# Performance work log

Hardware: AMD Instinct MI355X
Metric: run time of the kernel (lower is better)

Reference implementation:

```python
import jax, jax.numpy as jnp
import numpy as np

B, N, D, H = 4, 2048, 128, 8
DFF = 4 * D
EPS = 1e-5


def _mha(q, k, v, wq, bq, wk, bk, wv, bv, wo, bo):
    # q: [B, Nq, D], k/v: [B, Nk, D]
    b, nq, d = q.shape
    dh = d // H
    qh = (q @ wq + bq).reshape(b, nq, H, dh)
    kh = (k @ wk + bk).reshape(b, k.shape[1], H, dh)
    vh = (v @ wv + bv).reshape(b, v.shape[1], H, dh)
    scores = jnp.einsum('bqhd,bkhd->bhqk', qh, kh) / jnp.sqrt(jnp.float32(dh))
    attn = jax.nn.softmax(scores, axis=-1)
    out = jnp.einsum('bhqk,bkhd->bqhd', attn, vh).reshape(b, nq, d)
    return out @ wo + bo


def _ln(x, g, b):
    m = x.mean(-1, keepdims=True)
    v = x.var(-1, keepdims=True)
    return (x - m) / jnp.sqrt(v + EPS) * g + b


def setup_inputs() -> dict:
    key = jax.random.key(0)
    ks = jax.random.split(key, 20)
    w = lambda k, s: jax.random.normal(k, s, jnp.float32) * 0.02
    inp = {'h': jax.random.normal(ks[0], (B, N, D), jnp.float32)}
    inp['l_idx'] = jnp.arange(N // 2, dtype=jnp.int32)
    inp['b_idx'] = jnp.arange(N // 2, N, dtype=jnp.int32)
    i = 1
    for p in ('sa', 'l2b', 'b2l'):
        for proj in ('q', 'k', 'v', 'o'):
            inp[f'{p}_w{proj}'] = w(ks[i], (D, D)); i += 1
            inp[f'{p}_b{proj}'] = jnp.zeros((D,), jnp.float32)
    inp['ff_w1'] = w(ks[i], (D, DFF)); i += 1
    inp['ff_b1'] = jnp.zeros((DFF,), jnp.float32)
    inp['ff_w2'] = w(ks[i], (DFF, D)); i += 1
    inp['ff_b2'] = jnp.zeros((D,), jnp.float32)
    inp['n1_g'] = jnp.ones((D,), jnp.float32)
    inp['n1_b'] = jnp.zeros((D,), jnp.float32)
    inp['n2_g'] = jnp.ones((D,), jnp.float32)
    inp['n2_b'] = jnp.zeros((D,), jnp.float32)
    return inp


def reference(h, l_idx, b_idx,
              sa_wq, sa_bq, sa_wk, sa_bk, sa_wv, sa_bv, sa_wo, sa_bo,
              l2b_wq, l2b_bq, l2b_wk, l2b_bk, l2b_wv, l2b_bv, l2b_wo, l2b_bo,
              b2l_wq, b2l_bq, b2l_wk, b2l_bk, b2l_wv, b2l_bv, b2l_wo, b2l_bo,
              ff_w1, ff_b1, ff_w2, ff_b2, n1_g, n1_b, n2_g, n2_b):
    # Self-attention over all nodes.
    h_sa = _mha(h, h, h, sa_wq, sa_bq, sa_wk, sa_bk, sa_wv, sa_bv, sa_wo, sa_bo)
    # Gather node-type subsets, cross-attend, scatter into a zero buffer.
    h_l = h[:, l_idx]  # [B, Nl, D]
    h_b = h[:, b_idx]  # [B, Nb, D]
    out_l = _mha(h_l, h_b, h_b, l2b_wq, l2b_bq, l2b_wk, l2b_bk, l2b_wv, l2b_bv, l2b_wo, l2b_bo)
    out_b = _mha(h_b, h_l, h_l, b2l_wq, b2l_bq, b2l_wk, b2l_bk, b2l_wv, b2l_bv, b2l_wo, b2l_bo)
    h_het = jnp.zeros_like(h).at[:, l_idx].set(out_l).at[:, b_idx].set(out_b)
    x = _ln(h + h_sa + h_het, n1_g, n1_b)
    x = jnp.nan_to_num(x, nan=0.0)
    ff = jnp.maximum(x @ ff_w1 + ff_b1, 0.0) @ ff_w2 + ff_b2
    x = _ln(x + ff, n2_g, n2_b)
    return jnp.nan_to_num(x, nan=0.0)
```

## Files before the change

### kernel.cpp

```cpp
#include <hip/hip_runtime.h>

typedef unsigned short u16;
typedef short s16x4 __attribute__((ext_vector_type(4)));
typedef short short8 __attribute__((ext_vector_type(8)));
typedef __bf16 bf16x8 __attribute__((ext_vector_type(8)));
typedef float f32x4 __attribute__((ext_vector_type(4)));
typedef float f32x2 __attribute__((ext_vector_type(2)));
typedef float f32x16 __attribute__((ext_vector_type(16)));

#define DEV static __device__ __forceinline__

DEV u16 f2b(float f){
  union { float f; unsigned u; } v; v.f = f;
  return (u16)((v.u + 0x7fffu + ((v.u >> 16) & 1u)) >> 16);
}

DEV f32x4 mfma16(short8 a, short8 b, f32x4 c){
  return __builtin_amdgcn_mfma_f32_16x16x32_bf16(
      __builtin_bit_cast(bf16x8, a), __builtin_bit_cast(bf16x8, b), c, 0, 0, 0);
}

DEV f32x16 mfma32(short8 a, short8 b, f32x16 c){
  return __builtin_amdgcn_mfma_f32_32x32x16_bf16(
      __builtin_bit_cast(bf16x8, a), __builtin_bit_cast(bf16x8, b), c, 0, 0, 0);
}

DEV short8 ld8(const u16* p){ return *(const short8*)p; }

#if __has_builtin(__builtin_amdgcn_exp2f)
DEV float fexp2(float x){ return __builtin_amdgcn_exp2f(x); }
#else
DEV float fexp2(float x){ return exp2f(x); }
#endif

#define LOG2E 1.44269504088896341f

struct WConvArgs { const float* w[12]; const float* w1; const float* w2; const float* h; u16* dst; u16* hb; };
__global__ __launch_bounds__(256) void k_convert_w(WConvArgs a){
  int i = blockIdx.x*256 + threadIdx.x;
  if (i >= 1376256) return;
  if (i >= 327680){ int j = i - 327680; a.hb[j] = f2b(a.h[j]); return; }
  float v;
  if (i < 196608){ int w = i >> 14, rem = i & 16383, c = rem >> 7, k = rem & 127; v = a.w[w][k*128 + c]; }
  else if (i < 262144){ int rem = i - 196608, c = rem >> 7, k = rem & 127; v = a.w1[k*512 + c]; }
  else { int rem = i - 262144, c = rem >> 9, k = rem & 511; v = a.w2[k*128 + c]; }
  a.dst[i] = f2b(v);
}

struct ProjDesc {
  const u16* Wt; const float* bias; u16* dst;
  int lg_rpb, row_off, vtrans, tile_end; float scale;
};
struct ProjArgs { ProjDesc d[9]; const u16* X; };
__global__ __launch_bounds__(256) void k_qkv(ProjArgs A){
  int wave = (blockIdx.x << 2) + (threadIdx.x >> 6);
  int lane = threadIdx.x & 63;
  int j = 0, base = 0;
  #pragma unroll
  for (int t = 0; t < 8; ++t)
    if (wave >= A.d[t].tile_end){ j = t + 1; base = A.d[t].tile_end; }
  ProjDesc d = A.d[j];
  int local = wave - base;
  int ch = local & 1, rt = local >> 1;
  int lrow = lane & 15, lgrp = lane >> 4, kb = lgrp << 3;
  int rpb_m1 = (1 << d.lg_rpb) - 1;
  int nq = rpb_m1 + 1;
  int rA = (rt << 5) + lrow, rB = rA + 16;
  int gA = ((rA >> d.lg_rpb) << 11) + (rA & rpb_m1) + d.row_off;
  int gB = ((rB >> d.lg_rpb) << 11) + (rB & rpb_m1) + d.row_off;
  const u16* xpA = A.X + (size_t)gA*128 + kb;
  const u16* xpB = A.X + (size_t)gB*128 + kb;
  short8 aA0 = ld8(xpA), aA1 = ld8(xpA+32), aA2 = ld8(xpA+64), aA3 = ld8(xpA+96);
  short8 aB0 = ld8(xpB), aB1 = ld8(xpB+32), aB2 = ld8(xpB+64), aB3 = ld8(xpB+96);
  int rr0base = rt << 5;
  int b_of = rr0base >> d.lg_rpb;
  int q0_ = rr0base & rpb_m1;
  int blk = q0_ >> 5;
  int lgrp2 = ((lgrp & 1) << 1) | (lgrp >> 1);
  #pragma unroll
  for (int cc = 0; cc < 4; ++cc){
    int c = (ch << 6) + (cc << 4) + lrow;
    const u16* wp = d.Wt + c*128 + kb;
    short8 w0 = ld8(wp), w1 = ld8(wp+32), w2 = ld8(wp+64), w3 = ld8(wp+96);
    f32x4 accA = {0.f,0.f,0.f,0.f}, accB = {0.f,0.f,0.f,0.f};
    accA = mfma16(aA0, w0, accA); accB = mfma16(aB0, w0, accB);
    accA = mfma16(aA1, w1, accA); accB = mfma16(aB1, w1, accB);
    accA = mfma16(aA2, w2, accA); accB = mfma16(aB2, w2, accB);
    accA = mfma16(aA3, w3, accA); accB = mfma16(aB3, w3, accB);
    float bv = d.bias[c];
    int hh = c >> 4, dd = c & 15;
    #pragma unroll
    for (int half = 0; half < 2; ++half){
      f32x4 acc = half ? accB : accA;
      if (d.vtrans){
        s16x4 ov;
        #pragma unroll
        for (int i = 0; i < 4; ++i) ov[i] = (short)f2b((acc[i] + bv) * d.scale);
        size_t off = ((size_t)((b_of*8 + hh)*(nq >> 5) + blk))*512 + dd*32 + half*16 + lgrp2*4;
        *(s16x4*)(d.dst + off) = ov;
      } else {
        #pragma unroll
        for (int i = 0; i < 4; ++i){
          int rr = (rt << 5) + half*16 + (lgrp << 2) + i;
          int b = rr >> d.lg_rpb, q = rr & rpb_m1;
          float val = (acc[i] + bv) * d.scale;
          size_t off = ((size_t)((b*8 + hh)*nq + q))*16 + dd;
          d.dst[off] = f2b(val);
        }
      }
    }
  }
}

struct AttnDesc { const u16* Q; const u16* K; const u16* Vt; u16* ctx; int Nq, Nk, lg_nqt, wave_end; };
struct AttnArgs { AttnDesc d[3]; };
__global__ __launch_bounds__(256, 4) void k_attn(AttnArgs A){
  int wid = threadIdx.x >> 6, lane = threadIdx.x & 63;
  int p = blockIdx.x;
  int lb;
  if (p < 512){ lb = (p & 7)*64 + (p >> 3); }
  else if (p < 768){ int q = p - 512; lb = 512 + (q & 7)*32 + (q >> 3); }
  else { int q = p - 768; lb = 768 + (q & 7)*32 + (q >> 3); }
  int wave = (lb << 2) + wid;
  int j = 0, base = 0;
  #pragma unroll
  for (int t = 0; t < 2; ++t)
    if (wave >= A.d[t].wave_end){ j = t + 1; base = A.d[t].wave_end; }
  AttnDesc d = A.d[j];
  int local = wave - base;
  int bh = local >> d.lg_nqt;
  int qt = local & ((1 << d.lg_nqt) - 1);
  int q0 = qt << 5;
  int lq = lane & 31, hi = lane >> 5;
  const u16* Qb = d.Q + (size_t)bh * d.Nq * 16;
  const u16* Kb = d.K + (size_t)bh * d.Nk * 16;
  const u16* Vb = d.Vt + (size_t)bh * 16 * d.Nk;
  short8 zs = {0,0,0,0,0,0,0,0};
  short8 ones = {0x3F80,0x3F80,0x3F80,0x3F80,0x3F80,0x3F80,0x3F80,0x3F80};
  short8 bq = ld8(Qb + (q0 + lq)*16 + hi*8);
  const u16* kp0 = Kb + lq*16 + hi*8;
  bool vload = lq < 16;
  bool vone  = lq == 16;
  const u16* vbase = Vb + (lq & 15)*32 + hi*8;
  f32x16 oA = {0.f,0.f,0.f,0.f,0.f,0.f,0.f,0.f,0.f,0.f,0.f,0.f,0.f,0.f,0.f,0.f};
  f32x16 oB = oA;
  f32x16 z16 = oA;
  int nk = d.Nk;
  for (int k0 = 0; k0 < nk; k0 += 64){
    short8 aK0 = ld8(kp0 + k0*16);
    short8 aK1 = ld8(kp0 + k0*16 + 512);
    short8 v0a, v1a, v0b, v1b;
    if (vload){
      const u16* vp = vbase + (size_t)(k0 >> 5)*512;
      v0a = ld8(vp);        v1a = ld8(vp + 16);
      v0b = ld8(vp + 512);  v1b = ld8(vp + 528);
    } else if (vone){ v0a = ones; v1a = ones; v0b = ones; v1b = ones; }
    else { v0a = zs; v1a = zs; v0b = zs; v1b = zs; }
    f32x16 sA = mfma32(aK0, bq, z16);
    f32x16 sB = mfma32(aK1, bq, z16);
    float pa[16], pb_[16];
    #pragma unroll
    for (int i = 0; i < 16; ++i){ pa[i] = fexp2(sA[i]); pb_[i] = fexp2(sB[i]); }
    bf16x8 a0, a1, b0, b1;
    #pragma unroll
    for (int i = 0; i < 8; ++i){
      a0[i] = (__bf16)pa[i]; a1[i] = (__bf16)pa[8+i];
      b0[i] = (__bf16)pb_[i]; b1[i] = (__bf16)pb_[8+i];
    }
    oA = mfma32(v0a, __builtin_bit_cast(short8, a0), oA);
    oA = mfma32(v1a, __builtin_bit_cast(short8, a1), oA);
    oB = mfma32(v0b, __builtin_bit_cast(short8, b0), oB);
    oB = mfma32(v1b, __builtin_bit_cast(short8, b1), oB);
  }
  f32x16 o = oA + oB;
  float l = o[8];
  l += __shfl_xor(l, 32);
  float invl = 1.f / l;
  int b = bh >> 3, h = bh & 7;
  u16* cb = d.ctx + ((size_t)(b*d.Nq + q0 + lq))*128 + h*16;
  s16x4 ov0, ov1;
  #pragma unroll
  for (int i = 0; i < 4; ++i){
    ov0[i] = (short)f2b(o[i]   * invl);
    ov1[i] = (short)f2b(o[4+i] * invl);
  }
  *(s16x4*)(cb + 4*hi)     = ov0;
  *(s16x4*)(cb + 8 + 4*hi) = ov1;
}

struct OProjArgs {
  const u16 *ctx_sa, *ctx_l, *ctx_b, *wo_sa, *wo_l, *wo_b;
  const float *bo_sa, *bo_l, *bo_b, *h;
  float* sum;
};
__global__ __launch_bounds__(256) void k_oproj(OProjArgs A){
  int wave = (blockIdx.x << 2) + (threadIdx.x >> 6);
  int lane = threadIdx.x & 63;
  int ct = wave & 1, rt = wave >> 1;
  int lq = lane & 15, grp = lane >> 4, kb = grp << 3;
  int r0 = rt << 4;
  int r = r0 + lq;
  int b = r >> 11, q = r & 2047;
  bool lo = (q & 1024) == 0;
  int qh = q & 1023;
  const u16* asa = A.ctx_sa + (size_t)r*128 + kb;
  const u16* ah  = (lo ? A.ctx_l : A.ctx_b) + ((size_t)(b*1024 + qh))*128 + kb;
  short8 as0 = ld8(asa), as1 = ld8(asa+32), as2 = ld8(asa+64), as3 = ld8(asa+96);
  short8 ah0 = ld8(ah),  ah1 = ld8(ah+32),  ah2 = ld8(ah+64),  ah3 = ld8(ah+96);
  const u16* wlo = lo ? A.wo_l : A.wo_b;
  const float* blo = lo ? A.bo_l : A.bo_b;
  #pragma unroll
  for (int cc = 0; cc < 4; ++cc){
    int c = (ct << 6) + (cc << 4) + lq;
    const u16* wsa = A.wo_sa + c*128 + kb;
    const u16* wh  = wlo + c*128 + kb;
    f32x4 acc = {0.f,0.f,0.f,0.f};
    acc = mfma16(as0, ld8(wsa),      acc);
    acc = mfma16(as1, ld8(wsa + 32), acc);
    acc = mfma16(as2, ld8(wsa + 64), acc);
    acc = mfma16(as3, ld8(wsa + 96), acc);
    acc = mfma16(ah0, ld8(wh),       acc);
    acc = mfma16(ah1, ld8(wh + 32),  acc);
    acc = mfma16(ah2, ld8(wh + 64),  acc);
    acc = mfma16(ah3, ld8(wh + 96),  acc);
    float bv = A.bo_sa[c] + blo[c];
    #pragma unroll
    for (int i = 0; i < 4; ++i){
      int rr = r0 + (grp << 2) + i;
      size_t off = (size_t)rr*128 + c;
      A.sum[off] = A.h[off] + acc[i] + bv;
    }
  }
}

__global__ __launch_bounds__(256) void k_ff1(const float* sum, const float* gam, const float* bet,
                                             const u16* w1t, const float* b1, u16* t, float* x){
  int wave = (blockIdx.x << 2) + (threadIdx.x >> 6);
  int lane = threadIdx.x & 63;
  int ch = wave & 7, rt = wave >> 3;
  int lrow = lane & 15, lgrp = lane >> 4, kb = lgrp << 3;
  int rA = (rt << 5) + lrow, rB = rA + 16;
  const float* spA = sum + (size_t)rA*128 + kb;
  const float* spB = sum + (size_t)rB*128 + kb;
  float va[32], vb[32];
  float sA = 0.f, qA = 0.f, sB = 0.f, qB = 0.f;
  #pragma unroll
  for (int f = 0; f < 4; ++f){
    f32x4 a0 = *(const f32x4*)(spA + f*32), a1 = *(const f32x4*)(spA + f*32 + 4);
    f32x4 b0 = *(const f32x4*)(spB + f*32), b1 = *(const f32x4*)(spB + f*32 + 4);
    #pragma unroll
    for (int i = 0; i < 4; ++i){
      va[f*8+i] = a0[i]; va[f*8+4+i] = a1[i];
      vb[f*8+i] = b0[i]; vb[f*8+4+i] = b1[i];
      sA += a0[i] + a1[i]; qA += a0[i]*a0[i] + a1[i]*a1[i];
      sB += b0[i] + b1[i]; qB += b0[i]*b0[i] + b1[i]*b1[i];
    }
  }
  sA += __shfl_xor(sA, 16); qA += __shfl_xor(qA, 16);
  sA += __shfl_xor(sA, 32); qA += __shfl_xor(qA, 32);
  sB += __shfl_xor(sB, 16); qB += __shfl_xor(qB, 16);
  sB += __shfl_xor(sB, 32); qB += __shfl_xor(qB, 32);
  float mA = sA * 0.0078125f, mB = sB * 0.0078125f;
  float rA_ = rsqrtf(fmaxf(qA * 0.0078125f - mA*mA, 0.f) + 1e-5f);
  float rB_ = rsqrtf(fmaxf(qB * 0.0078125f - mB*mB, 0.f) + 1e-5f);
  short8 afA[4], afB[4];
  #pragma unroll
  for (int f = 0; f < 4; ++f){
    f32x4 g0 = *(const f32x4*)(gam + f*32 + kb), g1 = *(const f32x4*)(gam + f*32 + kb + 4);
    f32x4 c0 = *(const f32x4*)(bet + f*32 + kb), c1 = *(const f32x4*)(bet + f*32 + kb + 4);
    f32x4 xa0, xa1, xb0, xb1;
    #pragma unroll
    for (int i = 0; i < 4; ++i){
      xa0[i] = (va[f*8+i]   - mA)*rA_*g0[i] + c0[i];
      xa1[i] = (va[f*8+4+i] - mA)*rA_*g1[i] + c1[i];
      xb0[i] = (vb[f*8+i]   - mB)*rB_*g0[i] + c0[i];
      xb1[i] = (vb[f*8+4+i] - mB)*rB_*g1[i] + c1[i];
      afA[f][i] = (short)f2b(xa0[i]); afA[f][4+i] = (short)f2b(xa1[i]);
      afB[f][i] = (short)f2b(xb0[i]); afB[f][4+i] = (short)f2b(xb1[i]);
    }
    if (ch == 0){
      *(f32x4*)(x + (size_t)rA*128 + f*32 + kb)     = xa0;
      *(f32x4*)(x + (size_t)rA*128 + f*32 + kb + 4) = xa1;
      *(f32x4*)(x + (size_t)rB*128 + f*32 + kb)     = xb0;
      *(f32x4*)(x + (size_t)rB*128 + f*32 + kb + 4) = xb1;
    }
  }
  #pragma unroll
  for (int cc = 0; cc < 4; ++cc){
    int c = (ch << 6) + (cc << 4) + lrow;
    const u16* wp = w1t + c*128 + kb;
    short8 w0 = ld8(wp), w1 = ld8(wp+32), w2 = ld8(wp+64), w3 = ld8(wp+96);
    f32x4 accA = {0.f,0.f,0.f,0.f}, accB = {0.f,0.f,0.f,0.f};
    accA = mfma16(afA[0], w0, accA); accB = mfma16(afB[0], w0, accB);
    accA = mfma16(afA[1], w1, accA); accB = mfma16(afB[1], w1, accB);
    accA = mfma16(afA[2], w2, accA); accB = mfma16(afB[2], w2, accB);
    accA = mfma16(afA[3], w3, accA); accB = mfma16(afB[3], w3, accB);
    float bv = b1[c];
    #pragma unroll
    for (int half = 0; half < 2; ++half){
      f32x4 acc = half ? accB : accA;
      #pragma unroll
      for (int i = 0; i < 4; ++i){
        int rr = (rt << 5) + half*16 + (lgrp << 2) + i;
        t[(size_t)rr*512 + c] = f2b(fmaxf(acc[i] + bv, 0.f));
      }
    }
  }
}

__global__ __launch_bounds__(64) void k_ff2ln(const u16* t, const u16* w2t, const float* b2,
                                              const float* x, const float* gam, const float* bet,
                                              float* out){
  int rt = blockIdx.x;
  int lane = threadIdx.x & 63;
  int lq = lane & 15, grp = lane >> 4, kb = grp << 3;
  int r0 = rt << 4;
  const u16* ap = t + (size_t)(r0 + lq)*512 + kb;
  short8 af[16];
  #pragma unroll
  for (int ks = 0; ks < 16; ++ks) af[ks] = ld8(ap + ks*32);
  float v[8][4];
  #pragma unroll
  for (int ct = 0; ct < 8; ++ct){
    int c = (ct << 4) + lq;
    const u16* wp = w2t + (size_t)c*512 + kb;
    f32x4 acc = {0.f,0.f,0.f,0.f};
    #pragma unroll
    for (int ks = 0; ks < 16; ++ks) acc = mfma16(af[ks], ld8(wp + ks*32), acc);
    float bv = b2[c];
    #pragma unroll
    for (int i = 0; i < 4; ++i){
      int rr = r0 + (grp << 2) + i;
      v[ct][i] = x[(size_t)rr*128 + c] + acc[i] + bv;
    }
  }
  float s[4], sq[4];
  #pragma unroll
  for (int i = 0; i < 4; ++i){
    float a = 0.f, b = 0.f;
    #pragma unroll
    for (int ct = 0; ct < 8; ++ct){ a += v[ct][i]; b += v[ct][i]*v[ct][i]; }
    s[i] = a; sq[i] = b;
  }
  #pragma unroll
  for (int d = 1; d < 16; d <<= 1){
    #pragma unroll
    for (int i = 0; i < 4; ++i){ s[i] += __shfl_xor(s[i], d); sq[i] += __shfl_xor(sq[i], d); }
  }
  float mean[4], rstd[4];
  #pragma unroll
  for (int i = 0; i < 4; ++i){
    mean[i] = s[i] * 0.0078125f;
    rstd[i] = rsqrtf(fmaxf(sq[i]*0.0078125f - mean[i]*mean[i], 0.f) + 1e-5f);
  }
  #pragma unroll
  for (int ct = 0; ct < 8; ++ct){
    int c = (ct << 4) + lq;
    float g = gam[c], be = bet[c];
    #pragma unroll
    for (int i = 0; i < 4; ++i){
      int rr = r0 + (grp << 2) + i;
      out[(size_t)rr*128 + c] = (v[ct][i] - mean[i])*rstd[i]*g + be;
    }
  }
}

extern "C" void kernel_launch(void* const* d_in, const int* in_sizes, int n_in,
                              void* d_out, int out_size, void* d_ws, size_t ws_size,
                              hipStream_t stream){
  const float* h      = (const float*)d_in[0];
  const float* sa_wq  = (const float*)d_in[3];  const float* sa_bq  = (const float*)d_in[4];
  const float* sa_wk  = (const float*)d_in[5];  const float* sa_bk  = (const float*)d_in[6];
  const float* sa_wv  = (const float*)d_in[7];  const float* sa_bv  = (const float*)d_in[8];
  const float* sa_wo  = (const float*)d_in[9];  const float* sa_bo  = (const float*)d_in[10];
  const float* l2b_wq = (const float*)d_in[11]; const float* l2b_bq = (const float*)d_in[12];
  const float* l2b_wk = (const float*)d_in[13]; const float* l2b_bk = (const float*)d_in[14];
  const float* l2b_wv = (const float*)d_in[15]; const float* l2b_bv = (const float*)d_in[16];
  const float* l2b_wo = (const float*)d_in[17]; const float* l2b_bo = (const float*)d_in[18];
  const float* b2l_wq = (const float*)d_in[19]; const float* b2l_bq = (const float*)d_in[20];
  const float* b2l_wk = (const float*)d_in[21]; const float* b2l_bk = (const float*)d_in[22];
  const float* b2l_wv = (const float*)d_in[23]; const float* b2l_bv = (const float*)d_in[24];
  const float* b2l_wo = (const float*)d_in[25]; const float* b2l_bo = (const float*)d_in[26];
  const float* ff_w1  = (const float*)d_in[27]; const float* ff_b1  = (const float*)d_in[28];
  const float* ff_w2  = (const float*)d_in[29]; const float* ff_b2  = (const float*)d_in[30];
  const float* n1_g   = (const float*)d_in[31]; const float* n1_b   = (const float*)d_in[32];
  const float* n2_g   = (const float*)d_in[33]; const float* n2_b   = (const float*)d_in[34];

  char* ws = (char*)d_ws;
  size_t off = 0;
  auto alloc = [&](size_t bytes)->char*{ char* p = ws + off; off += (bytes + 255) & ~(size_t)255; return p; };
  u16*   wt     = (u16*)alloc(327680*2);
  u16*   q_sa   = (u16*)alloc(2097152);
  u16*   k_sa   = (u16*)alloc(2097152);
  u16*   vt_sa  = (u16*)alloc(2097152);
  u16*   q_l    = (u16*)alloc(1048576);
  u16*   k_l    = (u16*)alloc(1048576);
  u16*   vt_l   = (u16*)alloc(1048576);
  u16*   q_b    = (u16*)alloc(1048576);
  u16*   k_b    = (u16*)alloc(1048576);
  u16*   vt_b   = (u16*)alloc(1048576);
  u16*   ctx_sa = (u16*)alloc(2097152);
  u16*   ctx_l  = (u16*)alloc(1048576);
  u16*   ctx_b  = (u16*)alloc(1048576);
  float* sum    = (float*)alloc(4194304);
  float* x      = (float*)alloc(4194304);
  u16*   tbuf   = (u16*)alloc(8388608);
  u16*   hb     = tbuf;
  if (off > ws_size) return;

  { WConvArgs a;
    const float* wlist[12] = {sa_wq,sa_wk,sa_wv,sa_wo,l2b_wq,l2b_wk,l2b_wv,l2b_wo,b2l_wq,b2l_wk,b2l_wv,b2l_wo};
    for (int i = 0; i < 12; ++i) a.w[i] = wlist[i];
    a.w1 = ff_w1; a.w2 = ff_w2; a.h = h; a.dst = wt; a.hb = hb;
    k_convert_w<<<5376, 256, 0, stream>>>(a);
  }

  const float QS = 0.25f * LOG2E;
  { ProjArgs a; a.X = hb;
    auto set = [&](int i, int widx, const float* bias, u16* dst, int lg, int offr, int vt, float sc, int end){
      a.d[i] = {wt + widx*16384, bias, dst, lg, offr, vt, end, sc}; };
    set(0, 0, sa_bq,  q_sa, 11,    0, 0, QS,    512);
    set(1, 1, sa_bk,  k_sa, 11,    0, 0, 1.f,  1024);
    set(2, 2, sa_bv, vt_sa, 11,    0, 1, 1.f,  1536);
    set(3, 4, l2b_bq,  q_l, 10,    0, 0, QS,   1792);
    set(4, 5, l2b_bk,  k_l, 10, 1024, 0, 1.f,  2048);
    set(5, 6, l2b_bv, vt_l, 10, 1024, 1, 1.f,  2304);
    set(6, 8, b2l_bq,  q_b, 10, 1024, 0, QS,   2560);
    set(7, 9, b2l_bk,  k_b, 10,    0, 0, 1.f,  2816);
    set(8,10, b2l_bv, vt_b, 10,    0, 1, 1.f,  3072);
    k_qkv<<<768, 256, 0, stream>>>(a);
  }

  { AttnArgs a;
    a.d[0] = {q_sa, k_sa, vt_sa, ctx_sa, 2048, 2048, 6, 2048};
    a.d[1] = {q_l,  k_l,  vt_l,  ctx_l,  1024, 1024, 5, 3072};
    a.d[2] = {q_b,  k_b,  vt_b,  ctx_b,  1024, 1024, 5, 4096};
    k_attn<<<1024, 256, 0, stream>>>(a);
  }

  { OProjArgs a;
    a.ctx_sa = ctx_sa; a.ctx_l = ctx_l; a.ctx_b = ctx_b;
    a.wo_sa = wt + 3*16384; a.wo_l = wt + 7*16384; a.wo_b = wt + 11*16384;
    a.bo_sa = sa_bo; a.bo_l = l2b_bo; a.bo_b = b2l_bo;
    a.h = h; a.sum = sum;
    k_oproj<<<256, 256, 0, stream>>>(a);
  }

  k_ff1<<<512, 256, 0, stream>>>(sum, n1_g, n1_b, wt + 196608, ff_b1, tbuf, x);
  k_ff2ln<<<512, 64, 0, stream>>>(tbuf, wt + 262144, ff_b2, x, n2_g, n2_b, (float*)d_out);
}
```

Baseline: 83.16 us.

## Fuse LayerNorm1 into output projection and store normalized activations as bf16

Measured after the change: 81.29 us. -2.3%, faster.

```diff
diff --git a/kernel.cpp b/kernel.cpp
--- a/kernel.cpp
+++ b/kernel.cpp
@@ -13,6 +13,10 @@
 DEV u16 f2b(float f){
   union { float f; unsigned u; } v; v.f = f;
   return (u16)((v.u + 0x7fffu + ((v.u >> 16) & 1u)) >> 16);
+}
+
+DEV float b2f(u16 u){
+  union { unsigned u; float f; } v; v.u = ((unsigned)u) << 16; return v.f;
 }
 
 DEV f32x4 mfma16(short8 a, short8 b, f32x4 c){
@@ -190,13 +194,13 @@
 
 struct OProjArgs {
   const u16 *ctx_sa, *ctx_l, *ctx_b, *wo_sa, *wo_l, *wo_b;
-  const float *bo_sa, *bo_l, *bo_b, *h;
-  float* sum;
+  const float *bo_sa, *bo_l, *bo_b, *h, *gam, *bet;
+  u16* xb;
 };
 __global__ __launch_bounds__(256) void k_oproj(OProjArgs A){
   int wave = (blockIdx.x << 2) + (threadIdx.x >> 6);
   int lane = threadIdx.x & 63;
-  int ct = wave & 1, rt = wave >> 1;
+  int rt = wave;
   int lq = lane & 15, grp = lane >> 4, kb = grp << 3;
   int r0 = rt << 4;
   int r = r0 + lq;
@@ -209,9 +213,10 @@
   short8 ah0 = ld8(ah),  ah1 = ld8(ah+32),  ah2 = ld8(ah+64),  ah3 = ld8(ah+96);
   const u16* wlo = lo ? A.wo_l : A.wo_b;
   const float* blo = lo ? A.bo_l : A.bo_b;
-  #pragma unroll
-  for (int cc = 0; cc < 4; ++cc){
-    int c = (ct << 6) + (cc << 4) + lq;
+  float v[8][4];
+  #pragma unroll
+  for (int ct = 0; ct < 8; ++ct){
+    int c = (ct << 4) + lq;
     const u16* wsa = A.wo_sa + c*128 + kb;
     const u16* wh  = wlo + c*128 + kb;
     f32x4 acc = {0.f,0.f,0.f,0.f};
@@ -227,74 +232,60 @@
     #pragma unroll
     for (int i = 0; i < 4; ++i){
       int rr = r0 + (grp << 2) + i;
-      size_t off = (size_t)rr*128 + c;
-      A.sum[off] = A.h[off] + acc[i] + bv;
-    }
-  }
-}
-
-__global__ __launch_bounds__(256) void k_ff1(const float* sum, const float* gam, const float* bet,
-                                             const u16* w1t, const float* b1, u16* t, float* x){
+      v[ct][i] = A.h[(size_t)rr*128 + c] + acc[i] + bv;
+    }
+  }
+  float s[4], sq[4];
+  #pragma unroll
+  for (int i = 0; i < 4; ++i){
+    float a = 0.f, bb = 0.f;
+    #pragma unroll
+    for (int ct = 0; ct < 8; ++ct){ a += v[ct][i]; bb += v[ct][i]*v[ct][i]; }
+    s[i] = a; sq[i] = bb;
+  }
+  #pragma unroll
+  for (int dd = 1; dd < 16; dd <<= 1){
+    #pragma unroll
+    for (int i = 0; i < 4; ++i){ s[i] += __shfl_xor(s[i], dd); sq[i] += __shfl_xor(sq[i], dd); }
+  }
+  float mean[4], rstd[4];
+  #pragma unroll
+  for (int i = 0; i < 4; ++i){
+    mean[i] = s[i] * 0.0078125f;
+    rstd[i] = rsqrtf(fmaxf(sq[i]*0.0078125f - mean[i]*mean[i], 0.f) + 1e-5f);
+  }
+  #pragma unroll
+  for (int ct = 0; ct < 8; ++ct){
+    int c = (ct << 4) + lq;
+    float g = A.gam[c], be = A.bet[c];
+    #pragma unroll
+    for (int i = 0; i < 4; ++i){
+      int rr = r0 + (grp << 2) + i;
+      A.xb[(size_t)rr*128 + c] = f2b((v[ct][i] - mean[i])*rstd[i]*g + be);
+    }
+  }
+}
+
+__global__ __launch_bounds__(256) void k_ff1(const u16* xb, const u16* w1t, const float* b1, u16* t){
   int wave = (blockIdx.x << 2) + (threadIdx.x >> 6);
   int lane = threadIdx.x & 63;
   int ch = wave & 7, rt = wave >> 3;
   int lrow = lane & 15, lgrp = lane >> 4, kb = lgrp << 3;
   int rA = (rt << 5) + lrow, rB = rA + 16;
-  const float* spA = sum + (size_t)rA*128 + kb;
-  const float* spB = sum + (size_t)rB*128 + kb;
-  float va[32], vb[32];
-  float sA = 0.f, qA = 0.f, sB = 0.f, qB = 0.f;
-  #pragma unroll
-  for (int f = 0; f < 4; ++f){
-    f32x4 a0 = *(const f32x4*)(spA + f*32), a1 = *(const f32x4*)(spA + f*32 + 4);
-    f32x4 b0 = *(const f32x4*)(spB + f*32), b1 = *(const f32x4*)(spB + f*32 + 4);
-    #pragma unroll
-    for (int i = 0; i < 4; ++i){
-      va[f*8+i] = a0[i]; va[f*8+4+i] = a1[i];
-      vb[f*8+i] = b0[i]; vb[f*8+4+i] = b1[i];
-      sA += a0[i] + a1[i]; qA += a0[i]*a0[i] + a1[i]*a1[i];
-      sB += b0[i] + b1[i]; qB += b0[i]*b0[i] + b1[i]*b1[i];
-    }
-  }
-  sA += __shfl_xor(sA, 16); qA += __shfl_xor(qA, 16);
-  sA += __shfl_xor(sA, 32); qA += __shfl_xor(qA, 32);
-  sB += __shfl_xor(sB, 16); qB += __shfl_xor(qB, 16);
-  sB += __shfl_xor(sB, 32); qB += __shfl_xor(qB, 32);
-  float mA = sA * 0.0078125f, mB = sB * 0.0078125f;
-  float rA_ = rsqrtf(fmaxf(qA * 0.0078125f - mA*mA, 0.f) + 1e-5f);
-  float rB_ = rsqrtf(fmaxf(qB * 0.0078125f - mB*mB, 0.f) + 1e-5f);
-  short8 afA[4], afB[4];
-  #pragma unroll
-  for (int f = 0; f < 4; ++f){
-    f32x4 g0 = *(const f32x4*)(gam + f*32 + kb), g1 = *(const f32x4*)(gam + f*32 + kb + 4);
-    f32x4 c0 = *(const f32x4*)(bet + f*32 + kb), c1 = *(const f32x4*)(bet + f*32 + kb + 4);
-    f32x4 xa0, xa1, xb0, xb1;
-    #pragma unroll
-    for (int i = 0; i < 4; ++i){
-      xa0[i] = (va[f*8+i]   - mA)*rA_*g0[i] + c0[i];
-      xa1[i] = (va[f*8+4+i] - mA)*rA_*g1[i] + c1[i];
-      xb0[i] = (vb[f*8+i]   - mB)*rB_*g0[i] + c0[i];
-      xb1[i] = (vb[f*8+4+i] - mB)*rB_*g1[i] + c1[i];
-      afA[f][i] = (short)f2b(xa0[i]); afA[f][4+i] = (short)f2b(xa1[i]);
-      afB[f][i] = (short)f2b(xb0[i]); afB[f][4+i] = (short)f2b(xb1[i]);
-    }
-    if (ch == 0){
-      *(f32x4*)(x + (size_t)rA*128 + f*32 + kb)     = xa0;
-      *(f32x4*)(x + (size_t)rA*128 + f*32 + kb + 4) = xa1;
-      *(f32x4*)(x + (size_t)rB*128 + f*32 + kb)     = xb0;
-      *(f32x4*)(x + (size_t)rB*128 + f*32 + kb + 4) = xb1;
-    }
-  }
+  const u16* xpA = xb + (size_t)rA*128 + kb;
+  const u16* xpB = xb + (size_t)rB*128 + kb;
+  short8 aA0 = ld8(xpA), aA1 = ld8(xpA+32), aA2 = ld8(xpA+64), aA3 = ld8(xpA+96);
+  short8 aB0 = ld8(xpB), aB1 = ld8(xpB+32), aB2 = ld8(xpB+64), aB3 = ld8(xpB+96);
   #pragma unroll
   for (int cc = 0; cc < 4; ++cc){
     int c = (ch << 6) + (cc << 4) + lrow;
     const u16* wp = w1t + c*128 + kb;
     short8 w0 = ld8(wp), w1 = ld8(wp+32), w2 = ld8(wp+64), w3 = ld8(wp+96);
     f32x4 accA = {0.f,0.f,0.f,0.f}, accB = {0.f,0.f,0.f,0.f};
-    accA = mfma16(afA[0], w0, accA); accB = mfma16(afB[0], w0, accB);
-    accA = mfma16(afA[1], w1, accA); accB = mfma16(afB[1], w1, accB);
-    accA = mfma16(afA[2], w2, accA); accB = mfma16(afB[2], w2, accB);
-    accA = mfma16(afA[3], w3, accA); accB = mfma16(afB[3], w3, accB);
+    accA = mfma16(aA0, w0, accA); accB = mfma16(aB0, w0, accB);
+    accA = mfma16(aA1, w1, accA); accB = mfma16(aB1, w1, accB);
+    accA = mfma16(aA2, w2, accA); accB = mfma16(aB2, w2, accB);
+    accA = mfma16(aA3, w3, accA); accB = mfma16(aB3, w3, accB);
     float bv = b1[c];
     #pragma unroll
     for (int half = 0; half < 2; ++half){
@@ -309,7 +300,7 @@
 }
 
 __global__ __launch_bounds__(64) void k_ff2ln(const u16* t, const u16* w2t, const float* b2,
-                                              const float* x, const float* gam, const float* bet,
+                                              const u16* xb, const float* gam, const float* bet,
                                               float* out){
   int rt = blockIdx.x;
   int lane = threadIdx.x & 63;
@@ -331,7 +322,7 @@
     #pragma unroll
     for (int i = 0; i < 4; ++i){
       int rr = r0 + (grp << 2) + i;
-      v[ct][i] = x[(size_t)rr*128 + c] + acc[i] + bv;
+      v[ct][i] = b2f(xb[(size_t)rr*128 + c]) + acc[i] + bv;
     }
   }
   float s[4], sq[4];
@@ -402,8 +393,7 @@
   u16*   ctx_sa = (u16*)alloc(2097152);
   u16*   ctx_l  = (u16*)alloc(1048576);
   u16*   ctx_b  = (u16*)alloc(1048576);
-  float* sum    = (float*)alloc(4194304);
-  float* x      = (float*)alloc(4194304);
+  u16*   xb     = (u16*)alloc(2097152);
   u16*   tbuf   = (u16*)alloc(8388608);
   u16*   hb     = tbuf;
   if (off > ws_size) return;
@@ -442,10 +432,10 @@
     a.ctx_sa = ctx_sa; a.ctx_l = ctx_l; a.ctx_b = ctx_b;
     a.wo_sa = wt + 3*16384; a.wo_l = wt + 7*16384; a.wo_b = wt + 11*16384;
     a.bo_sa = sa_bo; a.bo_l = l2b_bo; a.bo_b = b2l_bo;
-    a.h = h; a.sum = sum;
-    k_oproj<<<256, 256, 0, stream>>>(a);
-  }
-
-  k_ff1<<<512, 256, 0, stream>>>(sum, n1_g, n1_b, wt + 196608, ff_b1, tbuf, x);
-  k_ff2ln<<<512, 64, 0, stream>>>(tbuf, wt + 262144, ff_b2, x, n2_g, n2_b, (float*)d_out);
-}
+    a.h = h; a.gam = n1_g; a.bet = n1_b; a.xb = xb;
+    k_oproj<<<128, 256, 0, stream>>>(a);
+  }
+
+  k_ff1<<<512, 256, 0, stream>>>(xb, wt + 196608, ff_b1, tbuf);
+  k_ff2ln<<<512, 64, 0, stream>>>(tbuf, wt + 262144, ff_b2, xb, n2_g, n2_b, (float*)d_out);
+}
```
